# Performance work log

Hardware: AMD Instinct MI355X
Metric: run time of the kernel (lower is better)

The kernel has to match this reference:

```python
import jax, jax.numpy as jnp
import numpy as np

N = 2097152
D = 128
CLASSES = 1000


def setup_inputs() -> dict:
    key = jax.random.key(0)
    k1, k2 = jax.random.split(key)
    X = jax.random.normal(k1, (N, D), dtype=jnp.float32)
    labels = jax.random.randint(k2, (N,), 0, CLASSES, dtype=jnp.int64)
    return {"X": X, "labels": labels, "classes": CLASSES}


def reference(X, labels, classes):
    # DistributionTracker.forward: per-label scatter-add of
    #   count (num), sum(X) (miu accumulator), sum(X^2) (std accumulator)
    # Fused here as three segment_sums over the label axis.
    num = jax.ops.segment_sum(jnp.ones((X.shape[0],), dtype=X.dtype), labels,
                              num_segments=classes)          # (c,)
    miu = jax.ops.segment_sum(X, labels, num_segments=classes)       # (c, D)
    sqr = jax.ops.segment_sum(X * X, labels, num_segments=classes)   # (c, D)
    # Pack into a single (c, 1 + 2D) array: [num | sum(X) | sum(X^2)]
    return jnp.concatenate([num[:, None], miu, sqr], axis=1)
```

## Files before the change

kernel.cpp:

```cpp
#include <hip/hip_runtime.h>


constexpr int DIM    = 128;
constexpr int ROWLEN = 2 * DIM + 1;

__global__ void hist_kernel(const int* __restrict__ labels, int N, int classes,
                            unsigned* __restrict__ hist,
                            float* __restrict__ out, int out_total)
{
    for (int i = blockIdx.x * blockDim.x + threadIdx.x; i < out_total;
         i += gridDim.x * blockDim.x) out[i] = 0.0f;

    __shared__ unsigned lh[1024];
    for (int i = threadIdx.x; i < 1024; i += blockDim.x) lh[i] = 0;
    __syncthreads();
    for (int i = blockIdx.x * blockDim.x + threadIdx.x; i < N;
         i += gridDim.x * blockDim.x) {
        const unsigned l = (unsigned)labels[i];
        if (l < (unsigned)classes) atomicAdd(&lh[l], 1u);
    }
    __syncthreads();
    for (int c = threadIdx.x; c < classes; c += blockDim.x)
        if (lh[c]) atomicAdd(&hist[c], lh[c]);
}

__global__ void prefix_kernel(const unsigned* __restrict__ hist,
                              unsigned* __restrict__ off,
                              unsigned* __restrict__ cursor, int classes)
{
    __shared__ unsigned s[1024];
    const int tid = threadIdx.x;
    s[tid] = (tid < classes) ? hist[tid] : 0u;
    __syncthreads();
    for (int d = 1; d < 1024; d <<= 1) {
        unsigned v = (tid >= d) ? s[tid - d] : 0u;
        __syncthreads();
        s[tid] += v;
        __syncthreads();
    }
    if (tid == 0) { off[0] = 0; cursor[0] = 0; }
    if (tid < classes) {
        off[tid + 1] = s[tid];
        if (tid > 0) cursor[tid] = s[tid - 1];
    }
}

constexpr int SCAT_T  = 256;
constexpr int SCAT_IT = 16;

__global__ void scatter_kernel(const int* __restrict__ labels, int N, int classes,
                               unsigned* __restrict__ cursor,
                               unsigned* __restrict__ idx)
{
    __shared__ unsigned lh[1024], lbase[1024];
    const int tid  = threadIdx.x;
    const int tile = blockIdx.x * (SCAT_T * SCAT_IT);
    for (int i = tid; i < 1024; i += SCAT_T) lh[i] = 0;
    __syncthreads();

    int lab[SCAT_IT];
#pragma unroll
    for (int k = 0; k < SCAT_IT; ++k) {
        const int row = tile + k * SCAT_T + tid;
        lab[k] = -1;
        if (row < N) {
            const unsigned l = (unsigned)labels[row];
            if (l < (unsigned)classes) { lab[k] = (int)l; atomicAdd(&lh[l], 1u); }
        }
    }
    __syncthreads();
    for (int c = tid; c < classes; c += SCAT_T) {
        if (lh[c]) lbase[c] = atomicAdd(&cursor[c], lh[c]);
        lh[c] = 0;
    }
    __syncthreads();
#pragma unroll
    for (int k = 0; k < SCAT_IT; ++k) {
        if (lab[k] >= 0) {
            const unsigned l   = (unsigned)lab[k];
            const unsigned row = (unsigned)(tile + k * SCAT_T + tid);
            idx[lbase[l] + atomicAdd(&lh[l], 1u)] = row;
        }
    }
}

constexpr int SPLIT = 8;
constexpr int U     = 8;

__global__ __launch_bounds__(64)
void accum_kernel(const float* __restrict__ X,
                  const unsigned* __restrict__ gidx,
                  const unsigned* __restrict__ off,
                  float* __restrict__ out)
{
    const int c = blockIdx.x / SPLIT;
    const int h = blockIdx.x % SPLIT;
    const unsigned s   = off[c];
    const unsigned cnt = off[c + 1] - s;
    if (cnt == 0) return;
    const unsigned s_h = s + (unsigned)(((unsigned long long)cnt * h) / SPLIT);
    const unsigned e_h = s + (unsigned)(((unsigned long long)cnt * (h + 1)) / SPLIT);
    if (s_h >= e_h) return;

    const int lane = threadIdx.x;

    float2 m[U], q[U];
#pragma unroll
    for (int u = 0; u < U; ++u) {
        m[u].x = m[u].y = 0.0f; q[u].x = q[u].y = 0.0f;
    }

    unsigned p = s_h;
    for (; p + U <= e_h; p += U) {
        const float2* Xr[U];
#pragma unroll
        for (int u = 0; u < U; ++u) {
            const unsigned r = __builtin_amdgcn_readfirstlane(gidx[p + u]);
            Xr[u] = (const float2*)(X + (size_t)r * DIM);
        }
#pragma unroll
        for (int u = 0; u < U; ++u) {
            const float2 x = Xr[u][lane];
            m[u].x += x.x;                 m[u].y += x.y;
            q[u].x = fmaf(x.x, x.x, q[u].x); q[u].y = fmaf(x.y, x.y, q[u].y);
        }
    }
    for (; p < e_h; ++p) {
        const unsigned r = __builtin_amdgcn_readfirstlane(gidx[p]);
        const float2 x = ((const float2*)(X + (size_t)r * DIM))[lane];
        m[0].x += x.x;                 m[0].y += x.y;
        q[0].x = fmaf(x.x, x.x, q[0].x); q[0].y = fmaf(x.y, x.y, q[0].y);
    }

#pragma unroll
    for (int u = 1; u < U; ++u) {
        m[0].x += m[u].x; m[0].y += m[u].y;
        q[0].x += q[u].x; q[0].y += q[u].y;
    }

    float* po = out + (size_t)c * ROWLEN;
    unsafeAtomicAdd(po + 1   + 2 * lane, m[0].x);
    unsafeAtomicAdd(po + 2   + 2 * lane, m[0].y);
    unsafeAtomicAdd(po + 129 + 2 * lane, q[0].x);
    unsafeAtomicAdd(po + 130 + 2 * lane, q[0].y);
    if (lane == 0) unsafeAtomicAdd(po, (float)(e_h - s_h));
}

constexpr int FB_T = 512;
constexpr int FB_W = FB_T / 64;
constexpr int FB_CG = 63;

__global__ __launch_bounds__(FB_T, 2)
void fb_kernel(const float* __restrict__ X, const int* __restrict__ labels,
               float* __restrict__ out, int N, int classes, int rpc)
{
    __shared__ float part[FB_CG * ROWLEN];
    const int tid = threadIdx.x, lane = tid & 63, wid = tid >> 6;
    const int gbase = blockIdx.y * FB_CG;
    for (int i = tid; i < FB_CG * ROWLEN; i += FB_T) part[i] = 0.0f;
    __syncthreads();
    const long long row0 = (long long)blockIdx.x * rpc;
    int rows = rpc;
    if (row0 + rows > N) rows = (int)((long long)N - row0);
    for (int base = wid * 64; base < rows; base += FB_W * 64) {
        const int nb = min(64, rows - base);
        int lab = -1;
        if (lane < nb) lab = labels[row0 + base + lane];
        const int lc = lab - gbase;
        const bool in = (lab >= 0) && (lc >= 0) && (lc < FB_CG) && (lab < classes);
        unsigned long long mask = __ballot(in);
        while (mask) {
            const int j = __ffsll((long long)mask) - 1;
            mask &= mask - 1;
            const int cc = __shfl(lc, j);
            const size_t ridx = (size_t)(row0 + base + j) * DIM;
            const float x0 = X[ridx + lane];
            const float x1 = X[ridx + lane + 64];
            float* pp = &part[cc * ROWLEN];
            unsafeAtomicAdd(&pp[1 + lane], x0);
            unsafeAtomicAdd(&pp[65 + lane], x1);
            unsafeAtomicAdd(&pp[129 + lane], x0 * x0);
            unsafeAtomicAdd(&pp[193 + lane], x1 * x1);
            if (lane == 0) unsafeAtomicAdd(&pp[0], 1.0f);
        }
    }
    __syncthreads();
    const int cmax = min(FB_CG, classes - gbase);
    float* gout = out + (size_t)gbase * ROWLEN;
    for (int i = tid; i < cmax * ROWLEN; i += FB_T) {
        const float vv = part[i];
        if (vv != 0.0f) unsafeAtomicAdd(&gout[i], vv);
    }
}

extern "C" void kernel_launch(void* const* d_in, const int* in_sizes, int n_in,
                              void* d_out, int out_size, void* d_ws, size_t ws_size,
                              hipStream_t stream)
{
    const float* X      = (const float*)d_in[0];
    const int*   labels = (const int*)d_in[1];
    float*       out    = (float*)d_out;

    const int N       = in_sizes[1];
    const int classes = out_size / ROWLEN;

    const size_t need = 12288 + (size_t)N * 4;
    const bool fast = (ws_size >= need) && (classes <= 1024);

    if (fast) {
        unsigned* hist   = (unsigned*)d_ws;
        unsigned* off    = (unsigned*)((char*)d_ws + 4096);
        unsigned* cursor = (unsigned*)((char*)d_ws + 8192);
        unsigned* idx    = (unsigned*)((char*)d_ws + 12288);

        hipMemsetAsync(d_ws, 0, 4096, stream);
        hist_kernel<<<512, 256, 0, stream>>>(labels, N, classes, hist,
                                             out, out_size);
        prefix_kernel<<<1, 1024, 0, stream>>>(hist, off, cursor, classes);
        const int sblocks = (N + SCAT_T * SCAT_IT - 1) / (SCAT_T * SCAT_IT);
        scatter_kernel<<<sblocks, SCAT_T, 0, stream>>>(labels, N, classes,
                                                       cursor, idx);
        accum_kernel<<<classes * SPLIT, 64, 0, stream>>>(X, idx, off, out);
    } else {
        hipMemsetAsync(d_out, 0, (size_t)out_size * sizeof(float), stream);
        const int groups = (classes + FB_CG - 1) / FB_CG;
        const int target_chunks = 32;
        int rpc = (N + target_chunks - 1) / target_chunks;
        const int batch = FB_W * 64;
        rpc = ((rpc + batch - 1) / batch) * batch;
        const int chunks = (N + rpc - 1) / rpc;
        dim3 grid(chunks, groups);
        fb_kernel<<<grid, FB_T, 0, stream>>>(X, labels, out, N, classes, rpc);
    }
}
```

Measured before the change: 263.6 us.

## Replace global histogram atomics with per-block partials, vectorize label loads, halve SPLIT

```diff
diff --git a/kernel.cpp b/kernel.cpp
--- a/kernel.cpp
+++ b/kernel.cpp
@@ -4,33 +4,56 @@
 constexpr int DIM    = 128;
 constexpr int ROWLEN = 2 * DIM + 1;
 
-__global__ void hist_kernel(const int* __restrict__ labels, int N, int classes,
-                            unsigned* __restrict__ hist,
-                            float* __restrict__ out, int out_total)
-{
-    for (int i = blockIdx.x * blockDim.x + threadIdx.x; i < out_total;
-         i += gridDim.x * blockDim.x) out[i] = 0.0f;
+constexpr int HIST_B = 256;
+constexpr int HIST_T = 256;
+
+__global__ __launch_bounds__(HIST_T)
+void hist_kernel(const int* __restrict__ labels, int N, int classes,
+                 unsigned* __restrict__ hist_part,
+                 float* __restrict__ out, int out_total)
+{
+    for (int i = blockIdx.x * HIST_T + threadIdx.x; i < out_total;
+         i += HIST_B * HIST_T) out[i] = 0.0f;
 
     __shared__ unsigned lh[1024];
-    for (int i = threadIdx.x; i < 1024; i += blockDim.x) lh[i] = 0;
-    __syncthreads();
-    for (int i = blockIdx.x * blockDim.x + threadIdx.x; i < N;
-         i += gridDim.x * blockDim.x) {
+    for (int i = threadIdx.x; i < 1024; i += HIST_T) lh[i] = 0;
+    __syncthreads();
+
+    const int gtid = blockIdx.x * HIST_T + threadIdx.x;
+    const int gstr = HIST_B * HIST_T;
+    const int N4   = N >> 2;
+    const int4* l4 = (const int4*)labels;
+    for (int i = gtid; i < N4; i += gstr) {
+        const int4 v = l4[i];
+        if ((unsigned)v.x < (unsigned)classes) atomicAdd(&lh[v.x], 1u);
+        if ((unsigned)v.y < (unsigned)classes) atomicAdd(&lh[v.y], 1u);
+        if ((unsigned)v.z < (unsigned)classes) atomicAdd(&lh[v.z], 1u);
+        if ((unsigned)v.w < (unsigned)classes) atomicAdd(&lh[v.w], 1u);
+    }
+    for (int i = (N4 << 2) + gtid; i < N; i += gstr) {
         const unsigned l = (unsigned)labels[i];
         if (l < (unsigned)classes) atomicAdd(&lh[l], 1u);
     }
     __syncthreads();
-    for (int c = threadIdx.x; c < classes; c += blockDim.x)
-        if (lh[c]) atomicAdd(&hist[c], lh[c]);
-}
-
-__global__ void prefix_kernel(const unsigned* __restrict__ hist,
-                              unsigned* __restrict__ off,
-                              unsigned* __restrict__ cursor, int classes)
+    unsigned* hp = hist_part + (size_t)blockIdx.x * 1024;
+    for (int i = threadIdx.x; i < 1024; i += HIST_T) hp[i] = lh[i];
+}
+
+__global__ __launch_bounds__(1024)
+void prefix_kernel(const unsigned* __restrict__ hist_part,
+                   unsigned* __restrict__ off,
+                   unsigned* __restrict__ cursor, int classes)
 {
     __shared__ unsigned s[1024];
     const int tid = threadIdx.x;
-    s[tid] = (tid < classes) ? hist[tid] : 0u;
+    unsigned a0 = 0, a1 = 0, a2 = 0, a3 = 0;
+    for (int b = 0; b < HIST_B; b += 4) {
+        a0 += hist_part[(b + 0) * 1024 + tid];
+        a1 += hist_part[(b + 1) * 1024 + tid];
+        a2 += hist_part[(b + 2) * 1024 + tid];
+        a3 += hist_part[(b + 3) * 1024 + tid];
+    }
+    s[tid] = (tid < classes) ? (a0 + a1 + a2 + a3) : 0u;
     __syncthreads();
     for (int d = 1; d < 1024; d <<= 1) {
         unsigned v = (tid >= d) ? s[tid - d] : 0u;
@@ -48,9 +71,10 @@
 constexpr int SCAT_T  = 256;
 constexpr int SCAT_IT = 16;
 
-__global__ void scatter_kernel(const int* __restrict__ labels, int N, int classes,
-                               unsigned* __restrict__ cursor,
-                               unsigned* __restrict__ idx)
+__global__ __launch_bounds__(SCAT_T)
+void scatter_kernel(const int* __restrict__ labels, int N, int classes,
+                    unsigned* __restrict__ cursor,
+                    unsigned* __restrict__ idx)
 {
     __shared__ unsigned lh[1024], lbase[1024];
     const int tid  = threadIdx.x;
@@ -84,7 +108,7 @@
     }
 }
 
-constexpr int SPLIT = 8;
+constexpr int SPLIT = 4;
 constexpr int U     = 8;
 
 __global__ __launch_bounds__(64)
@@ -121,14 +145,14 @@
 #pragma unroll
         for (int u = 0; u < U; ++u) {
             const float2 x = Xr[u][lane];
-            m[u].x += x.x;                 m[u].y += x.y;
+            m[u].x += x.x;                   m[u].y += x.y;
             q[u].x = fmaf(x.x, x.x, q[u].x); q[u].y = fmaf(x.y, x.y, q[u].y);
         }
     }
     for (; p < e_h; ++p) {
         const unsigned r = __builtin_amdgcn_readfirstlane(gidx[p]);
         const float2 x = ((const float2*)(X + (size_t)r * DIM))[lane];
-        m[0].x += x.x;                 m[0].y += x.y;
+        m[0].x += x.x;                   m[0].y += x.y;
         q[0].x = fmaf(x.x, x.x, q[0].x); q[0].y = fmaf(x.y, x.y, q[0].y);
     }
 
@@ -204,19 +228,19 @@
     const int N       = in_sizes[1];
     const int classes = out_size / ROWLEN;
 
-    const size_t need = 12288 + (size_t)N * 4;
+    const size_t HP_BYTES = (size_t)HIST_B * 1024 * 4;
+    const size_t need = HP_BYTES + 16384 + (size_t)N * 4;
     const bool fast = (ws_size >= need) && (classes <= 1024);
 
     if (fast) {
-        unsigned* hist   = (unsigned*)d_ws;
-        unsigned* off    = (unsigned*)((char*)d_ws + 4096);
-        unsigned* cursor = (unsigned*)((char*)d_ws + 8192);
-        unsigned* idx    = (unsigned*)((char*)d_ws + 12288);
-
-        hipMemsetAsync(d_ws, 0, 4096, stream);
-        hist_kernel<<<512, 256, 0, stream>>>(labels, N, classes, hist,
-                                             out, out_size);
-        prefix_kernel<<<1, 1024, 0, stream>>>(hist, off, cursor, classes);
+        unsigned* hist_part = (unsigned*)d_ws;
+        unsigned* off    = (unsigned*)((char*)d_ws + HP_BYTES);
+        unsigned* cursor = (unsigned*)((char*)d_ws + HP_BYTES + 8192);
+        unsigned* idx    = (unsigned*)((char*)d_ws + HP_BYTES + 16384);
+
+        hist_kernel<<<HIST_B, HIST_T, 0, stream>>>(labels, N, classes,
+                                                   hist_part, out, out_size);
+        prefix_kernel<<<1, 1024, 0, stream>>>(hist_part, off, cursor, classes);
         const int sblocks = (N + SCAT_T * SCAT_IT - 1) / (SCAT_T * SCAT_IT);
         scatter_kernel<<<sblocks, SCAT_T, 0, stream>>>(labels, N, classes,
                                                        cursor, idx);
```

Result: faster. 245.5 us (median of 2 runs) (-6.9%).
